# Performance work log

Measured on AMD Instinct MI355X. Metric: run time of the kernel, lower is better.

Reference implementation:

```python
import jax, jax.numpy as jnp
import numpy as np

D_MODEL = 1024
N_HEADS = 16
HEAD_DIM = D_MODEL // N_HEADS
EPS = 1e-6


def setup_inputs() -> dict:
    key = jax.random.key(0)
    ks = jax.random.split(key, 5)
    b, s = 2, 2048
    x = jax.random.normal(ks[0], (b, s, D_MODEL), dtype=jnp.float32)
    scale = 1.0 / np.sqrt(D_MODEL)
    Wq = jax.random.normal(ks[1], (D_MODEL, D_MODEL), dtype=jnp.float32) * scale
    Wk = jax.random.normal(ks[2], (D_MODEL, D_MODEL), dtype=jnp.float32) * scale
    Wv = jax.random.normal(ks[3], (D_MODEL, D_MODEL), dtype=jnp.float32) * scale
    Wo = jax.random.normal(ks[4], (D_MODEL, D_MODEL), dtype=jnp.float32) * scale
    return {"x": x, "Wq": Wq, "Wk": Wk, "Wv": Wv, "Wo": Wo}


def _feature_map(t):
    return jax.nn.relu(t) + EPS


def reference(x, Wq, Wk, Wv, Wo):
    b, s, _ = x.shape
    # nn.Linear applies x @ W.T
    q = (x @ Wq.T).reshape(b, s, N_HEADS, HEAD_DIM)
    k = (x @ Wk.T).reshape(b, s, N_HEADS, HEAD_DIM)
    v = (x @ Wv.T).reshape(b, s, N_HEADS, HEAD_DIM)
    q = _feature_map(q).transpose(0, 2, 1, 3)  # bhsd
    k = _feature_map(k).transpose(0, 2, 1, 3)  # bhsd
    v = v.transpose(0, 2, 1, 3)                # bhsm
    # cumulative KV outer products: (b,h,s,d,m)
    kv = jnp.einsum('bhsd,bhsm->bhsdm', k, v)
    kv_cum = jnp.cumsum(kv, axis=2)
    out = jnp.einsum('bhsd,bhsdm->bhsm', q, kv_cum)
    k_cum = jnp.cumsum(k, axis=2)
    z = 1.0 / (jnp.einsum('bhsd,bhsd->bhs', q, k_cum) + EPS)
    out = out * z[..., None]
    out = out.transpose(0, 2, 1, 3).reshape(b, s, D_MODEL)
    return out @ Wo.T
```

## Files before the change

### kernel.cpp

```cpp
#include <hip/hip_runtime.h>

#define EPSF 1e-6f

typedef short bf16x8_t __attribute__((ext_vector_type(8)));
typedef float f32x4_t __attribute__((ext_vector_type(4)));

__device__ __forceinline__ ushort f2bf(float f) {
  union { float f; uint32_t u; } c; c.f = f;
  return (ushort)((c.u + 0x7FFFu + ((c.u >> 16) & 1u)) >> 16);
}
__device__ __forceinline__ float bf2f(ushort u) {
  union { uint32_t u; float f; } c; c.u = ((uint32_t)u) << 16;
  return c.f;
}

#define SWB(row, kbyte) (((row) << 7) + ((kbyte) ^ (((row) & 7) << 4)))

__global__ __launch_bounds__(256) void cvt5_kernel(
    const float4* __restrict__ x, const float4* __restrict__ wq,
    const float4* __restrict__ wk, const float4* __restrict__ wv,
    const float4* __restrict__ wo,
    ushort4* __restrict__ xb, ushort4* __restrict__ wqb,
    ushort4* __restrict__ wkb, ushort4* __restrict__ wvb,
    ushort4* __restrict__ wob)
{
  const int i = blockIdx.x * 256 + threadIdx.x;
  const float4* src; ushort4* dst; int off;
  if (i < (1 << 20)) { src = x; dst = xb; off = i; }
  else {
    const int j = i - (1 << 20);
    const int r = j >> 18;
    off = j & ((1 << 18) - 1);
    src = (r == 0) ? wq : (r == 1) ? wk : (r == 2) ? wv : wo;
    dst = (r == 0) ? wqb : (r == 1) ? wkb : (r == 2) ? wvb : wob;
  }
  const float4 v = src[off];
  ushort4 o;
  o.x = f2bf(v.x); o.y = f2bf(v.y); o.z = f2bf(v.z); o.w = f2bf(v.w);
  dst[off] = o;
}

template<int RELU, int OUT_BF16>
__device__ __forceinline__ void gemm_bt_mfma(
    const ushort* __restrict__ A, const ushort* __restrict__ B,
    void* __restrict__ C, const int K, const int N,
    const int row0, const int col0)
{
  __shared__ __align__(16) ushort As[128 * 32];
  __shared__ __align__(16) ushort Bs[128 * 32];
  const int tid = threadIdx.x;
  const int lane = tid & 63;
  const int wv = tid >> 6;
  const int wr = (wv >> 1) * 64;
  const int wc = (wv & 1) * 64;

  f32x4_t acc[4][4];
#pragma unroll
  for (int m = 0; m < 4; ++m)
#pragma unroll
    for (int n = 0; n < 4; ++n) acc[m][n] = (f32x4_t){0.f, 0.f, 0.f, 0.f};

  const int fr = lane & 15;
  const int kh = (lane >> 4) * 8;

  for (int k0 = 0; k0 < K; k0 += 32) {
    __syncthreads();
#pragma unroll
    for (int issue = 0; issue < 2; ++issue) {
      const int chunk = wv * 64 + lane + issue * 256;
      const int row = chunk >> 2;
      const int kp = chunk & 3;
      const ushort* gsrcA = A + (size_t)(row0 + row) * K + k0 + kp * 8;
      const ushort* gsrcB = B + (size_t)(col0 + row) * K + k0 + kp * 8;
      ushort* ldstA = As + (size_t)(wv * 64 + issue * 256) * 8;
      ushort* ldstB = Bs + (size_t)(wv * 64 + issue * 256) * 8;
      __builtin_amdgcn_global_load_lds(
          (const __attribute__((address_space(1))) void*)gsrcA,
          (__attribute__((address_space(3))) void*)ldstA, 16, 0, 0);
      __builtin_amdgcn_global_load_lds(
          (const __attribute__((address_space(1))) void*)gsrcB,
          (__attribute__((address_space(3))) void*)ldstB, 16, 0, 0);
    }
    __syncthreads();

    bf16x8_t af[4], bfr[4];
#pragma unroll
    for (int m = 0; m < 4; ++m)
      af[m] = *(const bf16x8_t*)&As[(size_t)(wr + m * 16 + fr) * 32 + kh];
#pragma unroll
    for (int n = 0; n < 4; ++n)
      bfr[n] = *(const bf16x8_t*)&Bs[(size_t)(wc + n * 16 + fr) * 32 + kh];
#pragma unroll
    for (int m = 0; m < 4; ++m)
#pragma unroll
      for (int n = 0; n < 4; ++n)
        acc[m][n] = __builtin_amdgcn_mfma_f32_16x16x32_bf16(
            af[m], bfr[n], acc[m][n], 0, 0, 0);
  }

  const int rq = (lane >> 4) * 4;
#pragma unroll
  for (int m = 0; m < 4; ++m) {
#pragma unroll
    for (int r = 0; r < 4; ++r) {
      const size_t grow = (size_t)(row0 + wr + m * 16 + rq + r);
#pragma unroll
      for (int n = 0; n < 4; ++n) {
        float val = acc[m][n][r];
        if (RELU) val = fmaxf(val, 0.f) + EPSF;
        const size_t gcol = (size_t)(col0 + wc + n * 16 + fr);
        if (OUT_BF16) ((ushort*)C)[grow * N + gcol] = f2bf(val);
        else          ((float*)C)[grow * N + gcol] = val;
      }
    }
  }
}

__global__ __launch_bounds__(256) void qkv_gemm_kernel(
    const ushort* __restrict__ xb,
    const ushort* __restrict__ wqb, const ushort* __restrict__ wkb,
    const ushort* __restrict__ wvb,
    ushort* __restrict__ q, ushort* __restrict__ k, ushort* __restrict__ v)
{
  const int which = blockIdx.y >> 3;
  const int bcol = blockIdx.y & 7;
  const ushort* B = (which == 0) ? wqb : (which == 1) ? wkb : wvb;
  ushort* C = (which == 0) ? q : (which == 1) ? k : v;
  if (which < 2)
    gemm_bt_mfma<1, 1>(xb, B, C, 1024, 1024, blockIdx.x * 128, bcol * 128);
  else
    gemm_bt_mfma<0, 1>(xb, B, C, 1024, 1024, blockIdx.x * 128, bcol * 128);
}

__global__ __launch_bounds__(256) void out_gemm_kernel(
    const ushort* __restrict__ at, const ushort* __restrict__ wob,
    float* __restrict__ out)
{
  gemm_bt_mfma<0, 0>(at, wob, out, 1024, 1024, blockIdx.x * 128, blockIdx.y * 128);
}


__global__ __launch_bounds__(256) void chunk_sums_kernel(
    const ushort* __restrict__ kbuf, const ushort* __restrict__ vbuf,
    float* __restrict__ kvsum, float* __restrict__ ksum)
{
  __shared__ __align__(16) ushort Kt[64 * 64];
  __shared__ __align__(16) ushort Vt[64 * 64];
  const int chunk = blockIdx.x;
  const int seq = blockIdx.y;
  const int b = seq >> 4, h = seq & 15;
  const int tid = threadIdx.x;
  const size_t base = ((size_t)b * 2048 + chunk * 64) * 1024 + h * 64;

#pragma unroll
  for (int r = 0; r < 2; ++r) {
    const int idx = tid + (r << 8);
    const int j = idx >> 3;
    const int e0 = (idx & 7) << 3;
    const bf16x8_t kv8 = *(const bf16x8_t*)(kbuf + base + (size_t)j * 1024 + e0);
    const bf16x8_t vv8 = *(const bf16x8_t*)(vbuf + base + (size_t)j * 1024 + e0);
#pragma unroll
    for (int t = 0; t < 8; ++t) {
      *(ushort*)((char*)Kt + SWB(e0 + t, j * 2)) = (ushort)kv8[t];
      *(ushort*)((char*)Vt + SWB(e0 + t, j * 2)) = (ushort)vv8[t];
    }
  }
  __syncthreads();

  if (tid < 64) {
    float s = 0.f;
#pragma unroll
    for (int g = 0; g < 8; ++g) {
      const bf16x8_t kr = *(const bf16x8_t*)((char*)Kt + SWB(tid, g * 16));
#pragma unroll
      for (int t = 0; t < 8; ++t) s += bf2f((ushort)kr[t]);
    }
    ksum[((size_t)seq * 32 + chunk) * 64 + tid] = s;
  }

  const int lane = tid & 63;
  const int wv = tid >> 6;
  const int wm = (wv >> 1) * 32;
  const int wd = (wv & 1) * 32;
  const int fr = lane & 15;
  const int khb = (lane >> 4) * 16;

  f32x4_t acc[2][2];
#pragma unroll
  for (int m = 0; m < 2; ++m)
#pragma unroll
    for (int n = 0; n < 2; ++n) acc[m][n] = (f32x4_t){0.f, 0.f, 0.f, 0.f};

#pragma unroll
  for (int kk = 0; kk < 2; ++kk) {
    bf16x8_t av[2], bk[2];
#pragma unroll
    for (int m = 0; m < 2; ++m)
      av[m] = *(const bf16x8_t*)((char*)Vt + SWB(wm + m * 16 + fr, kk * 64 + khb));
#pragma unroll
    for (int n = 0; n < 2; ++n)
      bk[n] = *(const bf16x8_t*)((char*)Kt + SWB(wd + n * 16 + fr, kk * 64 + khb));
#pragma unroll
    for (int m = 0; m < 2; ++m)
#pragma unroll
      for (int n = 0; n < 2; ++n)
        acc[m][n] = __builtin_amdgcn_mfma_f32_16x16x32_bf16(
            av[m], bk[n], acc[m][n], 0, 0, 0);
  }

  const size_t kvbase = ((size_t)seq * 32 + chunk) << 12;
  const int rq = (lane >> 4) * 4;
#pragma unroll
  for (int m = 0; m < 2; ++m)
#pragma unroll
    for (int r = 0; r < 4; ++r) {
      const int mrow = wm + m * 16 + rq + r;
#pragma unroll
      for (int n = 0; n < 2; ++n) {
        const int dcol = wd + n * 16 + fr;
        kvsum[kvbase + (size_t)mrow * 64 + dcol] = acc[m][n][r];
      }
    }
}

__global__ __launch_bounds__(256) void scan_kernel(
    float* __restrict__ kvsum, float* __restrict__ ksum)
{
  const int slice = blockIdx.x & 15;
  const int seq = blockIdx.x >> 4;
  const int e = slice * 256 + threadIdx.x;
  const size_t base = ((size_t)seq << 17) + e;
  float run = 0.f;
  for (int c = 0; c < 32; ++c) {
    const size_t idx = base + ((size_t)c << 12);
    const float t = kvsum[idx];
    kvsum[idx] = run;
    run += t;
  }
  if (slice == 0 && threadIdx.x < 64) {
    const size_t kb = (size_t)seq * 2048 + threadIdx.x;
    float run2 = 0.f;
    for (int c = 0; c < 32; ++c) {
      const float t = ksum[kb + (size_t)c * 64];
      ksum[kb + (size_t)c * 64] = run2;
      run2 += t;
    }
  }
}

__global__ __launch_bounds__(256) void attn_chunk_kernel(
    const ushort* __restrict__ qbuf, const ushort* __restrict__ kbuf,
    const ushort* __restrict__ vbuf, const float* __restrict__ kvsum,
    const float* __restrict__ ksum, ushort* __restrict__ attn)
{
  __shared__ __align__(16) ushort Qs[64 * 64];
  __shared__ __align__(16) ushort Ks[64 * 64];
  __shared__ __align__(16) ushort Vt[64 * 64];
  __shared__ __align__(16) ushort Pl[64 * 64];
  __shared__ float ksp[64];
  __shared__ float zinv[64];
  const int chunk = blockIdx.x;
  const int seq = blockIdx.y;
  const int b = seq >> 4, h = seq & 15;
  const int tid = threadIdx.x;
  const size_t base = ((size_t)b * 2048 + chunk * 64) * 1024 + h * 64;

#pragma unroll
  for (int r = 0; r < 2; ++r) {
    const int idx = tid + (r << 8);
    const int row = idx >> 3;
    const int e0 = (idx & 7) << 3;
    const int kb = e0 << 1;
    *(bf16x8_t*)((char*)Qs + SWB(row, kb)) =
        *(const bf16x8_t*)(qbuf + base + (size_t)row * 1024 + e0);
    *(bf16x8_t*)((char*)Ks + SWB(row, kb)) =
        *(const bf16x8_t*)(kbuf + base + (size_t)row * 1024 + e0);
    const bf16x8_t vv8 = *(const bf16x8_t*)(vbuf + base + (size_t)row * 1024 + e0);
#pragma unroll
    for (int t = 0; t < 8; ++t)
      *(ushort*)((char*)Vt + SWB(e0 + t, row * 2)) = (ushort)vv8[t];
  }
  if (tid < 64) ksp[tid] = ksum[((size_t)seq * 32 + chunk) * 64 + tid];
  __syncthreads();

  const int lane = tid & 63;
  const int wv = tid >> 6;
  const int wr = (wv >> 1) * 32;
  const int wc = (wv & 1) * 32;
  const int fr = lane & 15;
  const int khb = (lane >> 4) * 16;
  const int rq = (lane >> 4) * 4;

  f32x4_t sf[2][2];
#pragma unroll
  for (int m = 0; m < 2; ++m)
#pragma unroll
    for (int n = 0; n < 2; ++n) sf[m][n] = (f32x4_t){0.f, 0.f, 0.f, 0.f};
#pragma unroll
  for (int kk = 0; kk < 2; ++kk) {
    bf16x8_t aq[2], bk[2];
#pragma unroll
    for (int m = 0; m < 2; ++m)
      aq[m] = *(const bf16x8_t*)((char*)Qs + SWB(wr + m * 16 + fr, kk * 64 + khb));
#pragma unroll
    for (int n = 0; n < 2; ++n)
      bk[n] = *(const bf16x8_t*)((char*)Ks + SWB(wc + n * 16 + fr, kk * 64 + khb));
#pragma unroll
    for (int m = 0; m < 2; ++m)
#pragma unroll
      for (int n = 0; n < 2; ++n)
        sf[m][n] = __builtin_amdgcn_mfma_f32_16x16x32_bf16(
            aq[m], bk[n], sf[m][n], 0, 0, 0);
  }
  __syncthreads();

#pragma unroll
  for (int m = 0; m < 2; ++m)
#pragma unroll
    for (int r = 0; r < 4; ++r) {
      const int i = wr + m * 16 + rq + r;
#pragma unroll
      for (int n = 0; n < 2; ++n) {
        const int j = wc + n * 16 + fr;
        const float pv = (j <= i) ? sf[m][n][r] : 0.f;
        *(ushort*)((char*)Pl + SWB(i, j * 2)) = f2bf(pv);
      }
    }
  const size_t kvbase = ((size_t)seq * 32 + chunk) << 12;
#pragma unroll
  for (int r = 0; r < 2; ++r) {
    const int idx = tid + (r << 8);
    const int mrow = idx >> 3;
    const int d0 = (idx & 7) << 3;
    const float4 lo = *(const float4*)(kvsum + kvbase + (size_t)mrow * 64 + d0);
    const float4 hi = *(const float4*)(kvsum + kvbase + (size_t)mrow * 64 + d0 + 4);
    bf16x8_t kv8;
    kv8[0] = (short)f2bf(lo.x); kv8[1] = (short)f2bf(lo.y);
    kv8[2] = (short)f2bf(lo.z); kv8[3] = (short)f2bf(lo.w);
    kv8[4] = (short)f2bf(hi.x); kv8[5] = (short)f2bf(hi.y);
    kv8[6] = (short)f2bf(hi.z); kv8[7] = (short)f2bf(hi.w);
    *(bf16x8_t*)((char*)Ks + SWB(mrow, d0 << 1)) = kv8;
  }
  __syncthreads();

  if (tid < 64) {
    const int i = tid;
    float dsum = 0.f, ssum = 0.f;
#pragma unroll
    for (int g = 0; g < 8; ++g) {
      const bf16x8_t qr = *(const bf16x8_t*)((char*)Qs + SWB(i, g * 16));
      const bf16x8_t pr = *(const bf16x8_t*)((char*)Pl + SWB(i, g * 16));
#pragma unroll
      for (int t = 0; t < 8; ++t) {
        dsum = fmaf(bf2f((ushort)qr[t]), ksp[g * 8 + t], dsum);
        ssum += bf2f((ushort)pr[t]);
      }
    }
    zinv[i] = 1.f / (dsum + ssum + EPSF);
  }

  f32x4_t of[2][2];
#pragma unroll
  for (int m = 0; m < 2; ++m)
#pragma unroll
    for (int n = 0; n < 2; ++n) of[m][n] = (f32x4_t){0.f, 0.f, 0.f, 0.f};
#pragma unroll
  for (int kk = 0; kk < 2; ++kk) {
    bf16x8_t ap[2], bv[2];
#pragma unroll
    for (int m = 0; m < 2; ++m)
      ap[m] = *(const bf16x8_t*)((char*)Pl + SWB(wr + m * 16 + fr, kk * 64 + khb));
#pragma unroll
    for (int n = 0; n < 2; ++n)
      bv[n] = *(const bf16x8_t*)((char*)Vt + SWB(wc + n * 16 + fr, kk * 64 + khb));
#pragma unroll
    for (int m = 0; m < 2; ++m)
#pragma unroll
      for (int n = 0; n < 2; ++n)
        of[m][n] = __builtin_amdgcn_mfma_f32_16x16x32_bf16(
            ap[m], bv[n], of[m][n], 0, 0, 0);
  }
#pragma unroll
  for (int kk = 0; kk < 2; ++kk) {
    bf16x8_t aq[2], bkv[2];
#pragma unroll
    for (int m = 0; m < 2; ++m)
      aq[m] = *(const bf16x8_t*)((char*)Qs + SWB(wr + m * 16 + fr, kk * 64 + khb));
#pragma unroll
    for (int n = 0; n < 2; ++n)
      bkv[n] = *(const bf16x8_t*)((char*)Ks + SWB(wc + n * 16 + fr, kk * 64 + khb));
#pragma unroll
    for (int m = 0; m < 2; ++m)
#pragma unroll
      for (int n = 0; n < 2; ++n)
        of[m][n] = __builtin_amdgcn_mfma_f32_16x16x32_bf16(
            aq[m], bkv[n], of[m][n], 0, 0, 0);
  }
  __syncthreads();

#pragma unroll
  for (int m = 0; m < 2; ++m)
#pragma unroll
    for (int r = 0; r < 4; ++r) {
      const int i = wr + m * 16 + rq + r;
      const float z = zinv[i];
#pragma unroll
      for (int n = 0; n < 2; ++n) {
        const int mcol = wc + n * 16 + fr;
        attn[base + (size_t)i * 1024 + mcol] = f2bf(of[m][n][r] * z);
      }
    }
}

extern "C" void kernel_launch(void* const* d_in, const int* in_sizes, int n_in,
                              void* d_out, int out_size, void* d_ws, size_t ws_size,
                              hipStream_t stream)
{
  (void)in_sizes; (void)n_in; (void)out_size; (void)ws_size;
  const float* x  = (const float*)d_in[0];
  const float* Wq = (const float*)d_in[1];
  const float* Wk = (const float*)d_in[2];
  const float* Wv = (const float*)d_in[3];
  const float* Wo = (const float*)d_in[4];
  float* out = (float*)d_out;

  const size_t NM = (size_t)4096 * 1024;
  ushort* xb  = (ushort*)d_ws;
  ushort* wqb = xb + NM;
  ushort* wkb = wqb + (1 << 20);
  ushort* wvb = wkb + (1 << 20);
  ushort* wob = wvb + (1 << 20);
  ushort* qb  = wob + (1 << 20);
  ushort* kb  = qb + NM;
  ushort* vb  = kb + NM;
  ushort* at  = vb + NM;
  float*  ksm = (float*)(at + NM);
  float*  kvs = (float*)d_out;

  cvt5_kernel<<<8192, 256, 0, stream>>>(
      (const float4*)x, (const float4*)Wq, (const float4*)Wk,
      (const float4*)Wv, (const float4*)Wo,
      (ushort4*)xb, (ushort4*)wqb, (ushort4*)wkb, (ushort4*)wvb, (ushort4*)wob);
  qkv_gemm_kernel<<<dim3(32, 24), 256, 0, stream>>>(xb, wqb, wkb, wvb, qb, kb, vb);
  chunk_sums_kernel<<<dim3(32, 32), 256, 0, stream>>>(kb, vb, kvs, ksm);
  scan_kernel<<<512, 256, 0, stream>>>(kvs, ksm);
  attn_chunk_kernel<<<dim3(32, 32), 256, 0, stream>>>(qb, kb, vb, kvs, ksm, at);
  out_gemm_kernel<<<dim3(32, 8), 256, 0, stream>>>(at, wob, out);
}
```

Measured before the change: 168.0 us.

## Swizzle GEMM LDS tiles, split-K output GEMM with atomics, prefetch scan loads

The GEMM LDS tiles now use an XOR swizzle, applied on both the global-to-LDS copy and the fragment reads, to cut bank conflicts, and the MFMA block is wrapped in s_setprio. The output projection is split over K into two halves that atomically add into a zeroed output, doubling the grid from 256 to 512 blocks for better CU occupancy. This costs a memset and float atomics, and the summation order now varies between runs. The scan kernel loads all 32 values up front to expose memory-level parallelism, and the KV chunk sums move from the output buffer to workspace.

```diff
diff --git a/kernel.cpp b/kernel.cpp
--- a/kernel.cpp
+++ b/kernel.cpp
@@ -15,6 +15,7 @@
 }
 
 #define SWB(row, kbyte) (((row) << 7) + ((kbyte) ^ (((row) & 7) << 4)))
+#define SWB32(row, kbyte) (((row) << 6) + ((kbyte) ^ ((((row) >> 1) & 3) << 4)))
 
 __global__ __launch_bounds__(256) void cvt5_kernel(
     const float4* __restrict__ x, const float4* __restrict__ wq,
@@ -40,14 +41,15 @@
   dst[off] = o;
 }
 
-template<int RELU, int OUT_BF16>
+template<int RELU, int OUT_BF16, int ATOMIC>
 __device__ __forceinline__ void gemm_bt_mfma(
     const ushort* __restrict__ A, const ushort* __restrict__ B,
-    void* __restrict__ C, const int K, const int N,
-    const int row0, const int col0)
-{
-  __shared__ __align__(16) ushort As[128 * 32];
-  __shared__ __align__(16) ushort Bs[128 * 32];
+    void* __restrict__ C, const int K,
+    const int kbeg, const int kend,
+    const int N, const int row0, const int col0)
+{
+  __shared__ __align__(16) uint As[2048];
+  __shared__ __align__(16) uint Bs[2048];
   const int tid = threadIdx.x;
   const int lane = tid & 63;
   const int wv = tid >> 6;
@@ -61,41 +63,49 @@
     for (int n = 0; n < 4; ++n) acc[m][n] = (f32x4_t){0.f, 0.f, 0.f, 0.f};
 
   const int fr = lane & 15;
-  const int kh = (lane >> 4) * 8;
-
-  for (int k0 = 0; k0 < K; k0 += 32) {
+  const int kb = lane & 48;
+
+  int rowc[2], scol[2];
+#pragma unroll
+  for (int is = 0; is < 2; ++is) {
+    const int c = tid + is * 256;
+    rowc[is] = c >> 2;
+    scol[is] = ((c & 3) ^ ((rowc[is] >> 1) & 3)) << 3;
+  }
+  const int du0 = wv * 256;
+  const int du1 = wv * 256 + 1024;
+
+  for (int k0 = kbeg; k0 < kend; k0 += 32) {
     __syncthreads();
-#pragma unroll
-    for (int issue = 0; issue < 2; ++issue) {
-      const int chunk = wv * 64 + lane + issue * 256;
-      const int row = chunk >> 2;
-      const int kp = chunk & 3;
-      const ushort* gsrcA = A + (size_t)(row0 + row) * K + k0 + kp * 8;
-      const ushort* gsrcB = B + (size_t)(col0 + row) * K + k0 + kp * 8;
-      ushort* ldstA = As + (size_t)(wv * 64 + issue * 256) * 8;
-      ushort* ldstB = Bs + (size_t)(wv * 64 + issue * 256) * 8;
-      __builtin_amdgcn_global_load_lds(
-          (const __attribute__((address_space(1))) void*)gsrcA,
-          (__attribute__((address_space(3))) void*)ldstA, 16, 0, 0);
-      __builtin_amdgcn_global_load_lds(
-          (const __attribute__((address_space(1))) void*)gsrcB,
-          (__attribute__((address_space(3))) void*)ldstB, 16, 0, 0);
-    }
+    __builtin_amdgcn_global_load_lds(
+        (const __attribute__((address_space(1))) void*)(A + (size_t)(row0 + rowc[0]) * K + k0 + scol[0]),
+        (__attribute__((address_space(3))) void*)(As + du0), 16, 0, 0);
+    __builtin_amdgcn_global_load_lds(
+        (const __attribute__((address_space(1))) void*)(B + (size_t)(col0 + rowc[0]) * K + k0 + scol[0]),
+        (__attribute__((address_space(3))) void*)(Bs + du0), 16, 0, 0);
+    __builtin_amdgcn_global_load_lds(
+        (const __attribute__((address_space(1))) void*)(A + (size_t)(row0 + rowc[1]) * K + k0 + scol[1]),
+        (__attribute__((address_space(3))) void*)(As + du1), 16, 0, 0);
+    __builtin_amdgcn_global_load_lds(
+        (const __attribute__((address_space(1))) void*)(B + (size_t)(col0 + rowc[1]) * K + k0 + scol[1]),
+        (__attribute__((address_space(3))) void*)(Bs + du1), 16, 0, 0);
     __syncthreads();
 
     bf16x8_t af[4], bfr[4];
 #pragma unroll
     for (int m = 0; m < 4; ++m)
-      af[m] = *(const bf16x8_t*)&As[(size_t)(wr + m * 16 + fr) * 32 + kh];
+      af[m] = *(const bf16x8_t*)((const char*)As + SWB32(wr + m * 16 + fr, kb));
 #pragma unroll
     for (int n = 0; n < 4; ++n)
-      bfr[n] = *(const bf16x8_t*)&Bs[(size_t)(wc + n * 16 + fr) * 32 + kh];
+      bfr[n] = *(const bf16x8_t*)((const char*)Bs + SWB32(wc + n * 16 + fr, kb));
+    __builtin_amdgcn_s_setprio(1);
 #pragma unroll
     for (int m = 0; m < 4; ++m)
 #pragma unroll
       for (int n = 0; n < 4; ++n)
         acc[m][n] = __builtin_amdgcn_mfma_f32_16x16x32_bf16(
             af[m], bfr[n], acc[m][n], 0, 0, 0);
+    __builtin_amdgcn_s_setprio(0);
   }
 
   const int rq = (lane >> 4) * 4;
@@ -109,8 +119,9 @@
         float val = acc[m][n][r];
         if (RELU) val = fmaxf(val, 0.f) + EPSF;
         const size_t gcol = (size_t)(col0 + wc + n * 16 + fr);
-        if (OUT_BF16) ((ushort*)C)[grow * N + gcol] = f2bf(val);
-        else          ((float*)C)[grow * N + gcol] = val;
+        if (ATOMIC)        atomicAdd(&((float*)C)[grow * N + gcol], val);
+        else if (OUT_BF16) ((ushort*)C)[grow * N + gcol] = f2bf(val);
+        else               ((float*)C)[grow * N + gcol] = val;
       }
     }
   }
@@ -127,16 +138,20 @@
   const ushort* B = (which == 0) ? wqb : (which == 1) ? wkb : wvb;
   ushort* C = (which == 0) ? q : (which == 1) ? k : v;
   if (which < 2)
-    gemm_bt_mfma<1, 1>(xb, B, C, 1024, 1024, blockIdx.x * 128, bcol * 128);
+    gemm_bt_mfma<1, 1, 0>(xb, B, C, 1024, 0, 1024, 1024,
+                          blockIdx.x * 128, bcol * 128);
   else
-    gemm_bt_mfma<0, 1>(xb, B, C, 1024, 1024, blockIdx.x * 128, bcol * 128);
+    gemm_bt_mfma<0, 1, 0>(xb, B, C, 1024, 0, 1024, 1024,
+                          blockIdx.x * 128, bcol * 128);
 }
 
 __global__ __launch_bounds__(256) void out_gemm_kernel(
     const ushort* __restrict__ at, const ushort* __restrict__ wob,
     float* __restrict__ out)
 {
-  gemm_bt_mfma<0, 0>(at, wob, out, 1024, 1024, blockIdx.x * 128, blockIdx.y * 128);
+  const int kb0 = blockIdx.z * 512;
+  gemm_bt_mfma<0, 0, 1>(at, wob, out, 1024, kb0, kb0 + 512, 1024,
+                        blockIdx.x * 128, blockIdx.y * 128);
 }
 
 
@@ -144,8 +159,8 @@
     const ushort* __restrict__ kbuf, const ushort* __restrict__ vbuf,
     float* __restrict__ kvsum, float* __restrict__ ksum)
 {
-  __shared__ __align__(16) ushort Kt[64 * 64];
-  __shared__ __align__(16) ushort Vt[64 * 64];
+  __shared__ __align__(16) uint Kt[2048];
+  __shared__ __align__(16) uint Vt[2048];
   const int chunk = blockIdx.x;
   const int seq = blockIdx.y;
   const int b = seq >> 4, h = seq & 15;
@@ -230,18 +245,25 @@
   const int seq = blockIdx.x >> 4;
   const int e = slice * 256 + threadIdx.x;
   const size_t base = ((size_t)seq << 17) + e;
+  float vals[32];
+#pragma unroll
+  for (int c = 0; c < 32; ++c) vals[c] = kvsum[base + ((size_t)c << 12)];
   float run = 0.f;
+#pragma unroll
   for (int c = 0; c < 32; ++c) {
-    const size_t idx = base + ((size_t)c << 12);
-    const float t = kvsum[idx];
-    kvsum[idx] = run;
+    const float t = vals[c];
+    kvsum[base + ((size_t)c << 12)] = run;
     run += t;
   }
   if (slice == 0 && threadIdx.x < 64) {
     const size_t kb = (size_t)seq * 2048 + threadIdx.x;
+    float kv2[32];
+#pragma unroll
+    for (int c = 0; c < 32; ++c) kv2[c] = ksum[kb + (size_t)c * 64];
     float run2 = 0.f;
+#pragma unroll
     for (int c = 0; c < 32; ++c) {
-      const float t = ksum[kb + (size_t)c * 64];
+      const float t = kv2[c];
       ksum[kb + (size_t)c * 64] = run2;
       run2 += t;
     }
@@ -253,10 +275,10 @@
     const ushort* __restrict__ vbuf, const float* __restrict__ kvsum,
     const float* __restrict__ ksum, ushort* __restrict__ attn)
 {
-  __shared__ __align__(16) ushort Qs[64 * 64];
-  __shared__ __align__(16) ushort Ks[64 * 64];
-  __shared__ __align__(16) ushort Vt[64 * 64];
-  __shared__ __align__(16) ushort Pl[64 * 64];
+  __shared__ __align__(16) uint Qs[2048];
+  __shared__ __align__(16) uint Ks[2048];
+  __shared__ __align__(16) uint Vt[2048];
+  __shared__ __align__(16) uint Pl[2048];
   __shared__ float ksp[64];
   __shared__ float zinv[64];
   const int chunk = blockIdx.x;
@@ -416,7 +438,7 @@
                               void* d_out, int out_size, void* d_ws, size_t ws_size,
                               hipStream_t stream)
 {
-  (void)in_sizes; (void)n_in; (void)out_size; (void)ws_size;
+  (void)in_sizes; (void)n_in; (void)ws_size;
   const float* x  = (const float*)d_in[0];
   const float* Wq = (const float*)d_in[1];
   const float* Wk = (const float*)d_in[2];
@@ -435,7 +457,9 @@
   ushort* vb  = kb + NM;
   ushort* at  = vb + NM;
   float*  ksm = (float*)(at + NM);
-  float*  kvs = (float*)d_out;
+  float*  kvs = ksm + 65536;
+
+  hipMemsetAsync(d_out, 0, (size_t)out_size * sizeof(float), stream);
 
   cvt5_kernel<<<8192, 256, 0, stream>>>(
       (const float4*)x, (const float4*)Wq, (const float4*)Wk,
@@ -445,5 +469,5 @@
   chunk_sums_kernel<<<dim3(32, 32), 256, 0, stream>>>(kb, vb, kvs, ksm);
   scan_kernel<<<512, 256, 0, stream>>>(kvs, ksm);
   attn_chunk_kernel<<<dim3(32, 32), 256, 0, stream>>>(qb, kb, vb, kvs, ksm, at);
-  out_gemm_kernel<<<dim3(32, 8), 256, 0, stream>>>(at, wob, out);
-}
+  out_gemm_kernel<<<dim3(32, 8, 2), 256, 0, stream>>>(at, wob, out);
+}
```

Result: slower. 203.5 us (+21.1%).
